# Kernel tuning notes

Measured on AMD Instinct MI355X. Metric: run time of the kernel, lower is better.

Reference implementation:

```python
import jax, jax.numpy as jnp
import numpy as np

# Dimensions: B batch, V variables per sample, VT table rows, F feature, E embed_dim,
# NH healpix adjacency width. N6/N5/N4 grid sizes per zoom; PF fine patch points.
B, V, VT, F, E, NH = 2, 4, 4, 128, 128, 7
N6, N5, N4 = 196608, 49152, 12288
PF = 32768
P5, P4 = PF // 4, PF // 16   # coarse patch sizes
O5, O4 = 4, 16               # fine points per coarse point (4**(zoom - zoom_proc))
BIG = 1e10
EPS = 1e-20


def setup_inputs() -> dict:
    key = jax.random.key(0)
    ks = jax.random.split(key, 13)
    return {
        "table6": jax.random.normal(ks[0], (VT, N6, F), jnp.float32) * 0.02,
        "table5": jax.random.normal(ks[1], (VT, N5, F), jnp.float32) * 0.02,
        "table4": jax.random.normal(ks[2], (VT, N4, F), jnp.float32) * 0.02,
        "W": jax.random.normal(ks[3], (F, E), jnp.float32) / np.float32(np.sqrt(F)),
        "b": jnp.zeros((E,), jnp.float32),
        "rel_dists5": jax.random.uniform(ks[4], (B, P5, O5, NH), jnp.float32, 0.01, 1.0),
        "rel_dists4": jax.random.uniform(ks[5], (B, P4, O4, NH), jnp.float32, 0.01, 1.0),
        "mask5": (jax.random.uniform(ks[6], (B, P5, NH)) < 0.05).astype(jnp.float32),
        "mask4": (jax.random.uniform(ks[7], (B, P4, NH)) < 0.05).astype(jnp.float32),
        "var_indices": jax.random.randint(ks[8], (B, V), 0, VT),
        "idx6": jax.random.randint(ks[9], (B, PF), 0, N6),
        "nh_idx5": jax.random.randint(ks[10], (B, P5 * NH), 0, N5),
        "nh_idx4": jax.random.randint(ks[11], (B, P4 * NH), 0, N4),
    }


def _gather(table, var_idx, idx):
    # Fused get_embeddings_from_var_idx + get_patch / get_patch_nh:
    # out[b, v, p, f] = table[var_idx[b, v], idx[b, p], f]  -> [B, V, P, F]
    return table[var_idx[:, :, None], idx[:, None, :]]


def _interpolate(e, rel_dists, mask, n_out):
    # Embedding_interpolator: distance-weighted nh interpolation.
    # e: [B, V, Pc*NH, F]; rel_dists: [B, Pc, n_out, NH]; mask: [B, Pc, NH]
    rd = rel_dists + mask[:, :, None, :] * BIG  # invalid neighbors -> ~zero weight
    w = 1.0 / (EPS + rd)
    w = w / w.sum(axis=-1, keepdims=True)       # [B, Pc, n_out, NH]
    bsz, v, _, f = e.shape
    pc = rel_dists.shape[1]
    e = e.reshape(bsz, v, pc, NH, f)
    out = jnp.einsum('bvpnf,bpon->bvpof', e, w)  # [B, V, Pc, n_out, F]
    return out.reshape(bsz, v, 1, pc * n_out, f)  # t-dim unsqueezed, [B,V,1,PF,F]


def reference(table6, table5, table4, W, b, rel_dists5, rel_dists4,
              mask5, mask4, var_indices, idx6, nh_idx5, nh_idx4):
    # zoom_proc == zoom (6): patch gather + linear layer
    e6 = _gather(table6, var_indices, idx6)          # [B, V, PF, F]
    e6 = (e6 @ W + b)[:, :, None, :, :]              # [B, V, 1, PF, E]
    # zoom_proc 5 < zoom: nh gather + polar-distance interpolation (4 fine per coarse)
    e5 = _interpolate(_gather(table5, var_indices, nh_idx5), rel_dists5, mask5, O5)
    # zoom_proc 4 < zoom: nh gather + interpolation (16 fine per coarse)
    e4 = _interpolate(_gather(table4, var_indices, nh_idx4), rel_dists4, mask4, O4)
    return e6 + e5 + e4                               # [B, V, 1, PF, E]
```

## Files before the change

kernel.cpp:

```cpp
#include <hip/hip_runtime.h>
#include <cstdint>
#include <cstddef>

#define Bb 2
#define Vv 4
#define VTt 4
#define Ff 128
#define Ee 128
#define NHh 7
#define N6c 196608
#define N5c 49152
#define N4c 12288
#define PFc 32768
#define P5c 8192
#define P4c 2048
#define O5c 4
#define O4c 16
#define GRP 4

typedef __attribute__((ext_vector_type(8))) short short8;
typedef __attribute__((ext_vector_type(4))) float f32x4;
typedef __attribute__((ext_vector_type(2))) float f32x2;
typedef unsigned short u16;

__device__ __forceinline__ u16 f2bf(float f){
  union { float f; unsigned int i; } c; c.f = f;
  unsigned int x = c.i;
  return (u16)((x + 0x7fffu + ((x >> 16) & 1u)) >> 16);
}

__global__ void setup_kernel(const float* __restrict__ W, u16* __restrict__ wsw){
  int tid = blockIdx.x * 256 + threadIdx.x;
  if (tid < 16384){
    int j = tid & 7, lane = (tid >> 3) & 63, kk = (tid >> 9) & 3, nt = tid >> 11;
    int f = kk * 32 + (lane >> 4) * 8 + j;
    int e = nt * 16 + (lane & 15);
    wsw[tid] = f2bf(W[f * Ee + e]);
  }
}

__device__ __forceinline__ void gload_lds16(const float* g, float* l){
  __builtin_amdgcn_global_load_lds(
      (const __attribute__((address_space(1))) unsigned int*)g,
      (__attribute__((address_space(3))) unsigned int*)l, 16, 0, 0);
}

#define BAR_CONSUME() asm volatile("s_waitcnt vmcnt(0) lgkmcnt(0)\n\ts_barrier" ::: "memory")
#define BAR_LDS()     asm volatile("s_waitcnt lgkmcnt(0)\n\ts_barrier" ::: "memory")

__launch_bounds__(256, 3)
__global__ void mg_kernel(
    const float* __restrict__ t6, const float* __restrict__ t5, const float* __restrict__ t4,
    const float* __restrict__ rel5, const float* __restrict__ rel4,
    const float* __restrict__ m5, const float* __restrict__ m4,
    const int* __restrict__ vidx, const int* __restrict__ idx6,
    const int* __restrict__ nh5, const int* __restrict__ nh4,
    const u16* __restrict__ wsw, const float* __restrict__ bias,
    float* __restrict__ out)
{
  __shared__ float sT5[2][28 * 128];
  __shared__ float sT4[2][7 * 128];
  __shared__ float sW5[16 * 8];
  __shared__ float sW4[16 * 8];
  __shared__ float sB[Ee];
  __shared__ float sOut[16 * 132];

  const int tid = threadIdx.x;
  const int lane = tid & 63;
  const int wid = tid >> 6;
  const int blk = blockIdx.x;
  const int bv = blk / (P4c / GRP);
  const int pbase = (blk % (P4c / GRP)) * GRP;
  const int v = bv % Vv, b = bv / Vv;
  const int vi = vidx[b * Vv + v];

  if (tid < Ee) sB[tid] = bias[tid];

  auto stage = [&](int pp, int buf){
    float* d5 = sT5[buf];
    for (int k = tid; k < 896; k += 256){
      int row = k >> 5, c = k & 31;
      int gi = nh5[b * (P5c * NHh) + (pp * 4 + row / 7) * NHh + (row % 7)];
      gload_lds16(t5 + ((size_t)vi * N5c + gi) * Ff + c * 4, d5 + k * 4);
    }
    if (tid < 224){
      int row = tid >> 5, c = tid & 31;
      int gi = nh4[b * (P4c * NHh) + pp * NHh + row];
      gload_lds16(t4 + ((size_t)vi * N4c + gi) * Ff + c * 4, sT4[buf] + tid * 4);
    }
  };

  stage(pbase, 0);

  short8 bfrag[2][4];
  const int ntb = wid * 2;
#pragma unroll
  for (int i = 0; i < 2; i++)
#pragma unroll
    for (int kk = 0; kk < 4; kk++)
      bfrag[i][kk] = *(const short8*)(wsw + (((ntb + i) * 4 + kk) * 64 + lane) * 8);

  const int m = lane & 15, q = lane >> 4;

  for (int g = 0; g < GRP; g++){
    const int pc4 = pbase + g;
    const int cur = g & 1;
    const float* sT5c = sT5[cur];
    const float* sT4c = sT4[cur];

    if (tid >= 128 && tid < 144){
      int t = tid - 128;
      float raw[7], s = 0.f;
#pragma unroll
      for (int n = 0; n < 7; n++){
        float rd = rel4[((b * P4c + pc4) * O4c + t) * NHh + n]
                 + m4[(b * P4c + pc4) * NHh + n] * 1e10f;
        raw[n] = 1.0f / (1e-20f + rd); s += raw[n];
      }
      float inv = 1.0f / s;
#pragma unroll
      for (int n = 0; n < 7; n++) sW4[t * 8 + n] = raw[n] * inv;
    } else if (tid >= 144 && tid < 160){
      int t = tid - 144;
      int pc5 = pc4 * 4 + (t >> 2), o = t & 3;
      float raw[7], s = 0.f;
#pragma unroll
      for (int n = 0; n < 7; n++){
        float rd = rel5[((b * P5c + pc5) * O5c + o) * NHh + n]
                 + m5[(b * P5c + pc5) * NHh + n] * 1e10f;
        raw[n] = 1.0f / (1e-20f + rd); s += raw[n];
      }
      float inv = 1.0f / s;
#pragma unroll
      for (int n = 0; n < 7; n++) sW5[t * 8 + n] = raw[n] * inv;
    }

    int rown = idx6[b * PFc + pc4 * 16 + m];
    const float* arow = t6 + ((size_t)vi * N6c + rown) * Ff + q * 8;
    short8 af[4];
#pragma unroll
    for (int kk = 0; kk < 4; kk++){
      f32x4 lo = *(const f32x4*)(arow + kk * 32);
      f32x4 hi = *(const f32x4*)(arow + kk * 32 + 4);
      short8 cv;
#pragma unroll
      for (int j = 0; j < 4; j++){
        cv[j]     = (short)f2bf(lo[j]);
        cv[j + 4] = (short)f2bf(hi[j]);
      }
      af[kk] = cv;
    }

    BAR_CONSUME();

    if (g + 1 < GRP) stage(pc4 + 1, cur ^ 1);

    f32x4 acc0 = {0.f, 0.f, 0.f, 0.f}, acc1 = {0.f, 0.f, 0.f, 0.f};
#pragma unroll
    for (int kk = 0; kk < 4; kk++){
      acc0 = __builtin_amdgcn_mfma_f32_16x16x32_bf16(af[kk], bfrag[0][kk], acc0, 0, 0, 0);
      acc1 = __builtin_amdgcn_mfma_f32_16x16x32_bf16(af[kk], bfrag[1][kk], acc1, 0, 0, 0);
    }

    for (int k = tid; k < 1024; k += 256){
      int t = k >> 6, ep = (k & 63) * 2;
      float v0 = sB[ep], v1 = sB[ep + 1];
      const float* w4p = sW4 + t * 8;
      const float* w5p = sW5 + t * 8;
      const float* b4 = sT4c + ep;
      const float* b5 = sT5c + (t >> 2) * 7 * 128 + ep;
#pragma unroll
      for (int n = 0; n < 7; n++){
        f32x2 a4 = *(const f32x2*)(b4 + n * 128);
        float w4 = w4p[n];
        v0 += w4 * a4[0]; v1 += w4 * a4[1];
        f32x2 a5 = *(const f32x2*)(b5 + n * 128);
        float w5 = w5p[n];
        v0 += w5 * a5[0]; v1 += w5 * a5[1];
      }
      sOut[t * 132 + ep]     = v0;
      sOut[t * 132 + ep + 1] = v1;
    }

    BAR_LDS();

    {
      int col = wid * 32 + m;
#pragma unroll
      for (int r = 0; r < 4; r++){
        int row = q * 4 + r;
        sOut[row * 132 + col]      += acc0[r];
        sOut[row * 132 + col + 16] += acc1[r];
      }
    }

    BAR_LDS();

    {
      int t = tid >> 4, c = (tid & 15) * 8;
      const float* sp = sOut + t * 132 + c;
      size_t obase = (((size_t)bv) * PFc + (size_t)pc4 * 16 + t) * Ee + c;
      f32x4 w0 = *(const f32x4*)(sp);
      f32x4 w1 = *(const f32x4*)(sp + 4);
      __builtin_nontemporal_store(w0, (f32x4*)(out + obase));
      __builtin_nontemporal_store(w1, (f32x4*)(out + obase + 4));
    }
  }
}

extern "C" void kernel_launch(void* const* d_in, const int* in_sizes, int n_in,
                              void* d_out, int out_size, void* d_ws, size_t ws_size,
                              hipStream_t stream){
  const float* t6   = (const float*)d_in[0];
  const float* t5   = (const float*)d_in[1];
  const float* t4   = (const float*)d_in[2];
  const float* W    = (const float*)d_in[3];
  const float* bias = (const float*)d_in[4];
  const float* rel5 = (const float*)d_in[5];
  const float* rel4 = (const float*)d_in[6];
  const float* m5   = (const float*)d_in[7];
  const float* m4   = (const float*)d_in[8];
  const int* vidx = (const int*)d_in[9];
  const int* idx6 = (const int*)d_in[10];
  const int* nh5  = (const int*)d_in[11];
  const int* nh4  = (const int*)d_in[12];

  u16* wsw = (u16*)d_ws;

  setup_kernel<<<64, 256, 0, stream>>>(W, wsw);

  int grid = (Bb * Vv * P4c) / GRP;
  mg_kernel<<<grid, 256, 0, stream>>>(t6, t5, t4, rel5, rel4, m5, m4,
                                      vidx, idx6, nh5, nh4, wsw, bias,
                                      (float*)d_out);
}
```

Baseline: 699.2 us.

## Deepen gather pipeline: prefetch indices, A rows, rel/mask into LDS; drop setup kernel

Restructures the per-group pipeline so neighbour indices are loaded two groups ahead and the t6 rows and rel-distance/mask data are prefetched one group ahead. The rel and mask data go straight to LDS via async loads, and the barrier waits only with vmcnt(2) so the register A-row loads can stay in flight. The separate weight-swizzle kernel is removed and each block converts W to bf16 fragments itself, the group size doubles to 8, and the interpolation loop is vectorised to float4 and fused with the bias and MFMA result write. This aims to hide gather latency and cut a launch, at the cost of more registers and redundant per-block W conversion.

New measurement: 773.5 us. 10.6% more time.

```diff
diff --git a/kernel.cpp b/kernel.cpp
--- a/kernel.cpp
+++ b/kernel.cpp
@@ -4,7 +4,6 @@
 
 #define Bb 2
 #define Vv 4
-#define VTt 4
 #define Ff 128
 #define Ee 128
 #define NHh 7
@@ -14,14 +13,19 @@
 #define PFc 32768
 #define P5c 8192
 #define P4c 2048
-#define O5c 4
-#define O4c 16
-#define GRP 4
+#define GRP 8
 
 typedef __attribute__((ext_vector_type(8))) short short8;
 typedef __attribute__((ext_vector_type(4))) float f32x4;
-typedef __attribute__((ext_vector_type(2))) float f32x2;
 typedef unsigned short u16;
+
+#define OFF_T5 0
+#define OFF_T4 3584
+#define OFF_R4 4480
+#define OFF_R5 4592
+#define OFF_M4 4704
+#define OFF_M5 4712
+#define BUFSZ  4752
 
 __device__ __forceinline__ u16 f2bf(float f){
   union { float f; unsigned int i; } c; c.f = f;
@@ -29,45 +33,40 @@
   return (u16)((x + 0x7fffu + ((x >> 16) & 1u)) >> 16);
 }
 
-__global__ void setup_kernel(const float* __restrict__ W, u16* __restrict__ wsw){
-  int tid = blockIdx.x * 256 + threadIdx.x;
-  if (tid < 16384){
-    int j = tid & 7, lane = (tid >> 3) & 63, kk = (tid >> 9) & 3, nt = tid >> 11;
-    int f = kk * 32 + (lane >> 4) * 8 + j;
-    int e = nt * 16 + (lane & 15);
-    wsw[tid] = f2bf(W[f * Ee + e]);
-  }
-}
-
-__device__ __forceinline__ void gload_lds16(const float* g, float* l){
+__device__ __forceinline__ void gld16(const float* g, float* l){
   __builtin_amdgcn_global_load_lds(
       (const __attribute__((address_space(1))) unsigned int*)g,
       (__attribute__((address_space(3))) unsigned int*)l, 16, 0, 0);
 }
-
-#define BAR_CONSUME() asm volatile("s_waitcnt vmcnt(0) lgkmcnt(0)\n\ts_barrier" ::: "memory")
-#define BAR_LDS()     asm volatile("s_waitcnt lgkmcnt(0)\n\ts_barrier" ::: "memory")
+__device__ __forceinline__ void gld4(const float* g, float* l){
+  __builtin_amdgcn_global_load_lds(
+      (const __attribute__((address_space(1))) unsigned int*)g,
+      (__attribute__((address_space(3))) unsigned int*)l, 4, 0, 0);
+}
+
+#define BARC() asm volatile("s_waitcnt vmcnt(2) lgkmcnt(0)\n\ts_barrier" ::: "memory")
+#define BARL() asm volatile("s_waitcnt lgkmcnt(0)\n\ts_barrier" ::: "memory")
 
 __launch_bounds__(256, 3)
 __global__ void mg_kernel(
     const float* __restrict__ t6, const float* __restrict__ t5, const float* __restrict__ t4,
+    const float* __restrict__ W, const float* __restrict__ bias,
     const float* __restrict__ rel5, const float* __restrict__ rel4,
-    const float* __restrict__ m5, const float* __restrict__ m4,
+    const float* __restrict__ m5g, const float* __restrict__ m4g,
     const int* __restrict__ vidx, const int* __restrict__ idx6,
     const int* __restrict__ nh5, const int* __restrict__ nh4,
-    const u16* __restrict__ wsw, const float* __restrict__ bias,
     float* __restrict__ out)
 {
-  __shared__ float sT5[2][28 * 128];
-  __shared__ float sT4[2][7 * 128];
+  __shared__ float sBuf[2][BUFSZ];
+  __shared__ float sW4[16 * 8];
   __shared__ float sW5[16 * 8];
-  __shared__ float sW4[16 * 8];
   __shared__ float sB[Ee];
   __shared__ float sOut[16 * 132];
 
   const int tid = threadIdx.x;
   const int lane = tid & 63;
   const int wid = tid >> 6;
+  const int m = lane & 15, q = lane >> 4;
   const int blk = blockIdx.x;
   const int bv = blk / (P4c / GRP);
   const int pbase = (blk % (P4c / GRP)) * GRP;
@@ -76,131 +75,177 @@
 
   if (tid < Ee) sB[tid] = bias[tid];
 
-  auto stage = [&](int pp, int buf){
-    float* d5 = sT5[buf];
-    for (int k = tid; k < 896; k += 256){
-      int row = k >> 5, c = k & 31;
-      int gi = nh5[b * (P5c * NHh) + (pp * 4 + row / 7) * NHh + (row % 7)];
-      gload_lds16(t5 + ((size_t)vi * N5c + gi) * Ff + c * 4, d5 + k * 4);
-    }
-    if (tid < 224){
-      int row = tid >> 5, c = tid & 31;
-      int gi = nh4[b * (P4c * NHh) + pp * NHh + row];
-      gload_lds16(t4 + ((size_t)vi * N4c + gi) * Ff + c * 4, sT4[buf] + tid * 4);
-    }
+  struct Pack { int id0, id1, id2, id3, id4, rowA; };
+
+  auto load_idx = [&](int pc) -> Pack {
+    Pack p;
+    int r0 = tid >> 5;
+    p.id0 = nh5[b * (P5c * NHh) + (pc * 4 + r0 / 7) * NHh + (r0 % 7)];
+    int r1 = (tid + 256) >> 5;
+    p.id1 = nh5[b * (P5c * NHh) + (pc * 4 + r1 / 7) * NHh + (r1 % 7)];
+    int r2 = (tid + 512) >> 5;
+    p.id2 = nh5[b * (P5c * NHh) + (pc * 4 + r2 / 7) * NHh + (r2 % 7)];
+    if (tid < 128){
+      int r3 = (tid + 768) >> 5;
+      p.id3 = nh5[b * (P5c * NHh) + (pc * 4 + r3 / 7) * NHh + (r3 % 7)];
+    } else {
+      p.id3 = nh4[b * (P4c * NHh) + pc * NHh + ((tid - 128) >> 5)];
+    }
+    p.id4 = (tid < 96) ? nh4[b * (P4c * NHh) + pc * NHh + ((128 + tid) >> 5)] : 0;
+    p.rowA = idx6[b * PFc + pc * 16 + m];
+    return p;
   };
 
-  stage(pbase, 0);
+  auto stage = [&](float* buf, const Pack& p, int pc){
+    const size_t b5 = (size_t)vi * N5c, b4 = (size_t)vi * N4c;
+    const int c4 = (tid & 31) * 4;
+    gld16(t5 + (b5 + p.id0) * Ff + c4, buf + OFF_T5 + tid * 4);
+    gld16(t5 + (b5 + p.id1) * Ff + c4, buf + OFF_T5 + (tid + 256) * 4);
+    gld16(t5 + (b5 + p.id2) * Ff + c4, buf + OFF_T5 + (tid + 512) * 4);
+    if (tid < 128)
+      gld16(t5 + (b5 + p.id3) * Ff + c4, buf + OFF_T5 + (tid + 768) * 4);
+    else
+      gld16(t4 + (b4 + p.id3) * Ff + c4, buf + OFF_T4 + (tid - 128) * 4);
+    if (tid < 96)
+      gld16(t4 + (b4 + p.id4) * Ff + c4, buf + OFF_T4 + (128 + tid) * 4);
+    else if (tid >= 128 && tid < 156)
+      gld16(rel4 + (size_t)(b * P4c + pc) * 112 + (tid - 128) * 4, buf + OFF_R4 + (tid - 128) * 4);
+    else if (tid >= 192 && tid < 220)
+      gld16(rel5 + (size_t)(b * P5c + pc * 4) * 28 + (tid - 192) * 4, buf + OFF_R5 + (tid - 192) * 4);
+    if (tid < 7)
+      gld4(m4g + (b * P4c + pc) * 7 + tid, buf + OFF_M4 + tid);
+    else if (tid >= 64 && tid < 92)
+      gld4(m5g + (b * P5c + pc * 4) * 7 + (tid - 64), buf + OFF_M5 + (tid - 64));
+  };
+
+  f32x4 ra[8];
+  auto issueA = [&](int rowA){
+    const float* arow = t6 + ((size_t)vi * N6c + rowA) * Ff + q * 8;
+#pragma unroll
+    for (int kk = 0; kk < 4; kk++){
+      ra[2 * kk]     = *(const f32x4*)(arow + kk * 32);
+      ra[2 * kk + 1] = *(const f32x4*)(arow + kk * 32 + 4);
+    }
+  };
+
+  Pack pk = load_idx(pbase);
+  stage((float*)sBuf[0], pk, pbase);
+  issueA(pk.rowA);
+  Pack pkn = load_idx(pbase + 1);
 
   short8 bfrag[2][4];
-  const int ntb = wid * 2;
-#pragma unroll
-  for (int i = 0; i < 2; i++)
-#pragma unroll
-    for (int kk = 0; kk < 4; kk++)
-      bfrag[i][kk] = *(const short8*)(wsw + (((ntb + i) * 4 + kk) * 64 + lane) * 8);
-
-  const int m = lane & 15, q = lane >> 4;
+  {
+    const int ntb = wid * 2;
+#pragma unroll
+    for (int i = 0; i < 2; i++)
+#pragma unroll
+      for (int kk = 0; kk < 4; kk++){
+        short8 tf;
+#pragma unroll
+        for (int j = 0; j < 8; j++)
+          tf[j] = (short)f2bf(W[(kk * 32 + q * 8 + j) * Ee + (ntb + i) * 16 + m]);
+        bfrag[i][kk] = tf;
+      }
+  }
 
   for (int g = 0; g < GRP; g++){
     const int pc4 = pbase + g;
     const int cur = g & 1;
-    const float* sT5c = sT5[cur];
-    const float* sT4c = sT4[cur];
-
-    if (tid >= 128 && tid < 144){
-      int t = tid - 128;
-      float raw[7], s = 0.f;
-#pragma unroll
-      for (int n = 0; n < 7; n++){
-        float rd = rel4[((b * P4c + pc4) * O4c + t) * NHh + n]
-                 + m4[(b * P4c + pc4) * NHh + n] * 1e10f;
-        raw[n] = 1.0f / (1e-20f + rd); s += raw[n];
-      }
-      float inv = 1.0f / s;
-#pragma unroll
-      for (int n = 0; n < 7; n++) sW4[t * 8 + n] = raw[n] * inv;
-    } else if (tid >= 144 && tid < 160){
-      int t = tid - 144;
-      int pc5 = pc4 * 4 + (t >> 2), o = t & 3;
-      float raw[7], s = 0.f;
-#pragma unroll
-      for (int n = 0; n < 7; n++){
-        float rd = rel5[((b * P5c + pc5) * O5c + o) * NHh + n]
-                 + m5[(b * P5c + pc5) * NHh + n] * 1e10f;
-        raw[n] = 1.0f / (1e-20f + rd); s += raw[n];
-      }
-      float inv = 1.0f / s;
-#pragma unroll
-      for (int n = 0; n < 7; n++) sW5[t * 8 + n] = raw[n] * inv;
-    }
-
-    int rown = idx6[b * PFc + pc4 * 16 + m];
-    const float* arow = t6 + ((size_t)vi * N6c + rown) * Ff + q * 8;
+    const float* bufc = sBuf[cur];
+
     short8 af[4];
 #pragma unroll
     for (int kk = 0; kk < 4; kk++){
-      f32x4 lo = *(const f32x4*)(arow + kk * 32);
-      f32x4 hi = *(const f32x4*)(arow + kk * 32 + 4);
+      f32x4 lo = ra[2 * kk], hi = ra[2 * kk + 1];
       short8 cv;
 #pragma unroll
-      for (int j = 0; j < 4; j++){
-        cv[j]     = (short)f2bf(lo[j]);
-        cv[j + 4] = (short)f2bf(hi[j]);
-      }
+      for (int j = 0; j < 4; j++){ cv[j] = (short)f2bf(lo[j]); cv[j + 4] = (short)f2bf(hi[j]); }
       af[kk] = cv;
     }
 
-    BAR_CONSUME();
-
-    if (g + 1 < GRP) stage(pc4 + 1, cur ^ 1);
-
-    f32x4 acc0 = {0.f, 0.f, 0.f, 0.f}, acc1 = {0.f, 0.f, 0.f, 0.f};
+    BARC();
+
+    if (g + 1 < GRP){
+      stage((float*)sBuf[cur ^ 1], pkn, pc4 + 1);
+      issueA(pkn.rowA);
+    }
+    if (g + 2 < GRP) pkn = load_idx(pc4 + 2);
+
+    f32x4 acc0 = {0.f,0.f,0.f,0.f}, acc1 = {0.f,0.f,0.f,0.f};
 #pragma unroll
     for (int kk = 0; kk < 4; kk++){
       acc0 = __builtin_amdgcn_mfma_f32_16x16x32_bf16(af[kk], bfrag[0][kk], acc0, 0, 0, 0);
       acc1 = __builtin_amdgcn_mfma_f32_16x16x32_bf16(af[kk], bfrag[1][kk], acc1, 0, 0, 0);
     }
 
-    for (int k = tid; k < 1024; k += 256){
-      int t = k >> 6, ep = (k & 63) * 2;
-      float v0 = sB[ep], v1 = sB[ep + 1];
+    {
+      int col = wid * 32 + m;
+#pragma unroll
+      for (int r = 0; r < 4; r++){
+        int row = q * 4 + r;
+        sOut[row * 132 + col]      = acc0[r] + sB[col];
+        sOut[row * 132 + col + 16] = acc1[r] + sB[col + 16];
+      }
+    }
+
+    if (tid >= 128 && tid < 144){
+      int t = tid - 128;
+      const float* r4l = bufc + OFF_R4 + t * 7;
+      const float* m4l = bufc + OFF_M4;
+      float raw[7], s = 0.f;
+#pragma unroll
+      for (int n = 0; n < 7; n++){
+        float rd = r4l[n] + m4l[n] * 1e10f;
+        raw[n] = 1.0f / (1e-20f + rd); s += raw[n];
+      }
+      float inv = 1.0f / s;
+#pragma unroll
+      for (int n = 0; n < 7; n++) sW4[t * 8 + n] = raw[n] * inv;
+    } else if (tid >= 144 && tid < 160){
+      int t = tid - 144, p5l = t >> 2, o = t & 3;
+      const float* r5l = bufc + OFF_R5 + p5l * 28 + o * 7;
+      const float* m5l = bufc + OFF_M5 + p5l * 7;
+      float raw[7], s = 0.f;
+#pragma unroll
+      for (int n = 0; n < 7; n++){
+        float rd = r5l[n] + m5l[n] * 1e10f;
+        raw[n] = 1.0f / (1e-20f + rd); s += raw[n];
+      }
+      float inv = 1.0f / s;
+#pragma unroll
+      for (int n = 0; n < 7; n++) sW5[t * 8 + n] = raw[n] * inv;
+    }
+
+    BARL();
+
+#pragma unroll
+    for (int ii = 0; ii < 2; ii++){
+      int k = tid + ii * 256;
+      int t = k >> 5, ep = (k & 31) * 4;
+      float* so = sOut + t * 132 + ep;
+      f32x4 vv = *(const f32x4*)so;
       const float* w4p = sW4 + t * 8;
       const float* w5p = sW5 + t * 8;
-      const float* b4 = sT4c + ep;
-      const float* b5 = sT5c + (t >> 2) * 7 * 128 + ep;
+      const float* p4 = bufc + OFF_T4 + ep;
+      const float* p5 = bufc + OFF_T5 + (t >> 2) * 896 + ep;
 #pragma unroll
       for (int n = 0; n < 7; n++){
-        f32x2 a4 = *(const f32x2*)(b4 + n * 128);
-        float w4 = w4p[n];
-        v0 += w4 * a4[0]; v1 += w4 * a4[1];
-        f32x2 a5 = *(const f32x2*)(b5 + n * 128);
-        float w5 = w5p[n];
-        v0 += w5 * a5[0]; v1 += w5 * a5[1];
-      }
-      sOut[t * 132 + ep]     = v0;
-      sOut[t * 132 + ep + 1] = v1;
-    }
-
-    BAR_LDS();
+        f32x4 a4 = *(const f32x4*)(p4 + n * 128);
+        f32x4 a5 = *(const f32x4*)(p5 + n * 128);
+        float w4 = w4p[n], w5 = w5p[n];
+#pragma unroll
+        for (int jj = 0; jj < 4; jj++) vv[jj] += w4 * a4[jj] + w5 * a5[jj];
+      }
+      *(f32x4*)so = vv;
+    }
+
+    BARL();
 
     {
-      int col = wid * 32 + m;
-#pragma unroll
-      for (int r = 0; r < 4; r++){
-        int row = q * 4 + r;
-        sOut[row * 132 + col]      += acc0[r];
-        sOut[row * 132 + col + 16] += acc1[r];
-      }
-    }
-
-    BAR_LDS();
-
-    {
-      int t = tid >> 4, c = (tid & 15) * 8;
-      const float* sp = sOut + t * 132 + c;
-      size_t obase = (((size_t)bv) * PFc + (size_t)pc4 * 16 + t) * Ee + c;
-      f32x4 w0 = *(const f32x4*)(sp);
+      int tr = tid >> 4, c = (tid & 15) * 8;
+      const float* sp = sOut + tr * 132 + c;
+      size_t obase = (((size_t)bv) * PFc + (size_t)pc4 * 16 + tr) * Ee + c;
+      f32x4 w0 = *(const f32x4*)sp;
       f32x4 w1 = *(const f32x4*)(sp + 4);
       __builtin_nontemporal_store(w0, (f32x4*)(out + obase));
       __builtin_nontemporal_store(w1, (f32x4*)(out + obase + 4));
@@ -225,12 +270,9 @@
   const int* nh5  = (const int*)d_in[11];
   const int* nh4  = (const int*)d_in[12];
 
-  u16* wsw = (u16*)d_ws;
-
-  setup_kernel<<<64, 256, 0, stream>>>(W, wsw);
+  (void)d_ws; (void)ws_size;
 
   int grid = (Bb * Vv * P4c) / GRP;
-  mg_kernel<<<grid, 256, 0, stream>>>(t6, t5, t4, rel5, rel4, m5, m4,
-                                      vidx, idx6, nh5, nh4, wsw, bias,
-                                      (float*)d_out);
-}
+  mg_kernel<<<grid, 256, 0, stream>>>(t6, t5, t4, W, bias, rel5, rel4, m5, m4,
+                                      vidx, idx6, nh5, nh4, (float*)d_out);
+}
```
